# Kernel optimization log

Hardware: AMD Instinct MI355X
Metric: run time of the kernel (lower is better)

The kernel has to match this reference:

```python
import jax, jax.numpy as jnp
import numpy as np

N, D, DB, E, H = 1024, 512, 64, 32768, 1024

def setup_inputs() -> dict:
    key = jax.random.key(0)
    k = jax.random.split(key, 6)
    object_feats = jax.random.normal(k[0], (N, D), dtype=jnp.float32)
    bboxes_embedding = jax.random.normal(k[1], (N, N, DB), dtype=jnp.float32)
    pairs = jax.random.randint(k[2], (E, 2), 0, N, dtype=jnp.int64)
    # Kaiming-normal-ish init for the two Linear layers
    W1 = jax.random.normal(k[3], (D + D + DB, H), dtype=jnp.float32) * np.sqrt(2.0 / (D + D + DB))
    b1 = jnp.zeros((H,), dtype=jnp.float32)
    W2 = jax.random.normal(k[4], (H, D), dtype=jnp.float32) * np.sqrt(2.0 / H)
    b2 = jnp.zeros((D,), dtype=jnp.float32)
    return {"object_feats": object_feats, "bboxes_embedding": bboxes_embedding,
            "pairs": pairs, "W1": W1, "b1": b1, "W2": W2, "b2": b2}

def reference(object_feats, bboxes_embedding, pairs, W1, b1, W2, b2):
    sub = pairs[:, 0]
    obj = pairs[:, 1]
    # gather pair features: [E, D] each, plus pairwise bbox embedding [E, DB]
    f_sub = object_feats[sub]
    f_obj = object_feats[obj]
    bb = bboxes_embedding[sub, obj]
    x = jnp.concatenate((f_sub, f_obj, bb), axis=1)  # [E, 2D+DB]
    h = jax.nn.relu(x @ W1 + b1)
    out = h @ W2 + b2  # [E, D]
    n = object_feats.shape[0]
    # scatter-mean into subject nodes; each node's own feature is included once,
    # so new_feat[i] = (object_feats[i] + sum_{pairs with sub==i} out) / (1 + count[i]).
    # Nodes with no incident pairs keep their original feature (count==0 -> identity).
    seg_sum = jax.ops.segment_sum(out, sub, num_segments=n)  # [N, D]
    count = jax.ops.segment_sum(jnp.ones((out.shape[0],), dtype=out.dtype), sub, num_segments=n)
    new_feats = (object_feats + seg_sum) / (1.0 + count)[:, None]
    return (new_feats, bboxes_embedding, pairs)
```

## Files before the change

kernel.cpp:

```cpp
#include <hip/hip_runtime.h>

#define N_OBJ 1024
#define E_P   32768

typedef float f32x4 __attribute__((ext_vector_type(4)));
typedef short bf16x8 __attribute__((ext_vector_type(8)));
typedef unsigned short u16x4 __attribute__((ext_vector_type(4)));

__device__ __forceinline__ unsigned short f2bf(float f) {
    unsigned u = __float_as_uint(f);
    u = u + 0x7FFFu + ((u >> 16) & 1u);
    return (unsigned short)(u >> 16);
}

#define CP_OFF_PREP 0
#define CP_LEN_PREP 2097152
#define CP_OFF_PRE  (CP_OFF_PREP + CP_LEN_PREP)
#define CP_LEN_PRE  1048576
#define CP_OFF_PQ   (CP_OFF_PRE + CP_LEN_PRE)
#define CP_LEN_PQ   3145728
#define CP_OFF_SEG  (CP_OFF_PQ + CP_LEN_PQ)
#define CP_LEN_SEG  5242880
#define CP_OFF_OUT  (CP_OFF_SEG + CP_LEN_SEG)
#define CP_LEN_OUT  5242880

__device__ __forceinline__ void copy_role(const float4* __restrict__ src,
                                          float4* __restrict__ dst,
                                          int off, int len, int nblocks, int cb) {
    int i = off + cb * 256 + threadIdx.x;
    int end = off + len;
    int stride = nblocks * 256;
    for (; i < end; i += stride) dst[i] = src[i];
}

__global__ __launch_bounds__(256) void k_prep(const float* __restrict__ W1,
                                              const float* __restrict__ W2,
                                              const float* __restrict__ feats,
                                              unsigned short* __restrict__ w1pqT,
                                              unsigned short* __restrict__ w1cT,
                                              unsigned short* __restrict__ w2T,
                                              unsigned short* __restrict__ featsb,
                                              const float4* __restrict__ csrc,
                                              float4* __restrict__ cdst) {
    int bid = blockIdx.x;
    if ((bid % 3) == 2) { copy_role(csrc, cdst, CP_OFF_PREP, CP_LEN_PREP, 928, bid / 3); return; }
    int job = (bid / 3) * 2 + (bid % 3);
    int tid = threadIdx.x;
    if (job >= 1600) {
        int base = (job - 1600) * 2048 + tid * 8;
        float4 v0 = *(const float4*)&feats[base];
        float4 v1 = *(const float4*)&feats[base + 4];
        u16x4 o0 = { f2bf(v0.x), f2bf(v0.y), f2bf(v0.z), f2bf(v0.w) };
        u16x4 o1 = { f2bf(v1.x), f2bf(v1.y), f2bf(v1.z), f2bf(v1.w) };
        *(u16x4*)&featsb[base] = o0;
        *(u16x4*)&featsb[base + 4] = o1;
        return;
    }
    const float* in; unsigned short* out;
    int LDI, LDO, r0, c0, nbase, kbase;
    if (job < 1024) {
        int t = job; r0 = (t >> 5) * 32; c0 = (t & 31) * 32;
        in = W1; LDI = 1024; out = w1pqT; LDO = 512;
        nbase = c0 + (r0 >= 512 ? 1024 : 0); kbase = r0 & 511;
    } else if (job < 1088) {
        int t = job - 1024; r0 = 1024 + (t >> 5) * 32; c0 = (t & 31) * 32;
        in = W1; LDI = 1024; out = w1cT; LDO = 64;
        nbase = c0; kbase = r0 - 1024;
    } else {
        int t = job - 1088; r0 = (t >> 4) * 32; c0 = (t & 15) * 32;
        in = W2; LDI = 512; out = w2T; LDO = 1024;
        nbase = c0; kbase = r0;
    }
    __shared__ float lds[32][33];
    int ti = tid >> 3, tj = (tid & 7) * 4;
    float4 v = *(const float4*)&in[(size_t)(r0 + ti) * LDI + c0 + tj];
    lds[ti][tj] = v.x; lds[ti][tj + 1] = v.y; lds[ti][tj + 2] = v.z; lds[ti][tj + 3] = v.w;
    __syncthreads();
    int oc = tid >> 3, oj = (tid & 7) * 4;
    u16x4 o = { f2bf(lds[oj][oc]), f2bf(lds[oj + 1][oc]), f2bf(lds[oj + 2][oc]), f2bf(lds[oj + 3][oc]) };
    *(u16x4*)&out[(size_t)(nbase + oc) * LDO + kbase + oj] = o;
}

__global__ __launch_bounds__(256) void k_pre(const int* __restrict__ pairs,
                                             float* __restrict__ out_pairs,
                                             int* __restrict__ counts,
                                             const float4* __restrict__ csrc,
                                             float4* __restrict__ cdst) {
    int bid = blockIdx.x;
    if ((bid % 3) < 2) { copy_role(csrc, cdst, CP_OFF_PRE, CP_LEN_PRE, 512, (bid / 3) * 2 + (bid % 3)); return; }
    int i = (bid / 3) * 256 + threadIdx.x;
    if (i < 2 * E_P) out_pairs[i] = (float)pairs[i];
    if (i < E_P) atomicAdd(&counts[pairs[2 * i]], 1);
}

__global__ __launch_bounds__(256) void k_scan(const int* __restrict__ counts,
                                              int* __restrict__ offsets,
                                              int* __restrict__ cursor,
                                              int* __restrict__ brec,
                                              int* __restrict__ bcnt) {
    __shared__ int buf[2][256];
    int tid = threadIdx.x;
    int c[4]; int s = 0;
    #pragma unroll
    for (int i = 0; i < 4; ++i) { c[i] = counts[tid * 4 + i]; s += c[i]; }
    buf[0][tid] = s;
    __syncthreads();
    int sel = 0;
    for (int d = 1; d < 256; d <<= 1) {
        int v = buf[sel][tid];
        if (tid >= d) v += buf[sel][tid - d];
        buf[sel ^ 1][tid] = v;
        sel ^= 1;
        __syncthreads();
    }
    int base = buf[sel][tid] - s;
    int run = base;
    #pragma unroll
    for (int i = 0; i < 4; ++i) {
        offsets[tid * 4 + i] = run;
        cursor[tid * 4 + i]  = run;
        run += c[i];
    }
    if (tid == 255) offsets[1024] = run;
    int nb[4]; int t = 0;
    #pragma unroll
    for (int i = 0; i < 4; ++i) { nb[i] = (c[i] + 15) >> 4; t += nb[i]; }
    __syncthreads();
    buf[0][tid] = t;
    __syncthreads();
    sel = 0;
    for (int d = 1; d < 256; d <<= 1) {
        int v = buf[sel][tid];
        if (tid >= d) v += buf[sel][tid - d];
        buf[sel ^ 1][tid] = v;
        sel ^= 1;
        __syncthreads();
    }
    int bpos = buf[sel][tid] - t;
    #pragma unroll
    for (int i = 0; i < 4; ++i) {
        int seg = tid * 4 + i;
        for (int k = 0; k < nb[i]; ++k) brec[bpos++] = (seg << 8) | k;
    }
    if (tid == 255) bcnt[0] = bpos;
}

__global__ __launch_bounds__(256) void k_pq(const unsigned short* __restrict__ featsb,
                                            const unsigned short* __restrict__ w1pqT,
                                            const float* __restrict__ b1,
                                            float* __restrict__ P, float* __restrict__ Q,
                                            const int* __restrict__ pairs,
                                            int* __restrict__ cursor,
                                            int* __restrict__ csr,
                                            const float4* __restrict__ csrc,
                                            float4* __restrict__ cdst) {
    int bid = blockIdx.x;
    if (bid >= 1536) {
        int e = (bid - 1536) * 256 + threadIdx.x;
        if (e < E_P) {
            int sidx = pairs[2 * e];
            int pos = atomicAdd(&cursor[sidx], 1);
            csr[pos] = e;
        }
        return;
    }
    if ((bid % 3) < 2) { copy_role(csrc, cdst, CP_OFF_PQ, CP_LEN_PQ, 1024, (bid / 3) * 2 + (bid % 3)); return; }
    int job = bid / 3;
    int m0 = (job >> 5) * 64, n0 = (job & 31) * 64;
    int tid = threadIdx.x, w = tid >> 6, l = tid & 63;
    int ln = l & 15, kb = (l >> 4) * 8;
    int row = m0 + w * 16 + ln;
    f32x4 acc[4] = {};
    for (int k0 = 0; k0 < 512; k0 += 32) {
        bf16x8 a = *(const bf16x8*)&featsb[(size_t)row * 512 + k0 + kb];
        #pragma unroll
        for (int f = 0; f < 4; ++f) {
            bf16x8 b = *(const bf16x8*)&w1pqT[(size_t)(n0 + f * 16 + ln) * 512 + k0 + kb];
            acc[f] = __builtin_amdgcn_mfma_f32_16x16x32_bf16(a, b, acc[f], 0, 0, 0);
        }
    }
    int mr = m0 + w * 16 + (l >> 4) * 4;
    if (n0 < 1024) {
        #pragma unroll
        for (int f = 0; f < 4; ++f) {
            int n = n0 + f * 16 + ln;
            float b1v = b1[n];
            #pragma unroll
            for (int r = 0; r < 4; ++r)
                P[(size_t)(mr + r) * 1024 + n] = acc[f][r] + b1v;
        }
    } else {
        #pragma unroll
        for (int f = 0; f < 4; ++f) {
            int n = n0 - 1024 + f * 16 + ln;
            #pragma unroll
            for (int r = 0; r < 4; ++r)
                Q[(size_t)(mr + r) * 1024 + n] = acc[f][r];
        }
    }
}

__global__ __launch_bounds__(256) void k_seg(const int* __restrict__ csr,
                                             const int* __restrict__ offsets,
                                             const int* __restrict__ brec,
                                             const int* __restrict__ bcnt,
                                             const int* __restrict__ pairs,
                                             const float* __restrict__ bb,
                                             const unsigned short* __restrict__ w1cT,
                                             const float* __restrict__ P,
                                             const float* __restrict__ Q,
                                             float* __restrict__ HS,
                                             const float4* __restrict__ csrc,
                                             float4* __restrict__ cdst) {
    int bid = blockIdx.x;
    if ((bid % 3) == 0) { copy_role(csrc, cdst, CP_OFF_SEG, CP_LEN_SEG, 1536, bid / 3); return; }
    int b = (bid / 3) * 2 + (bid % 3) - 1;
    if (b >= bcnt[0]) return;
    int rec = brec[b];
    int seg = rec >> 8, kchunk = rec & 255;
    int start = offsets[seg] + kchunk * 16;
    int end = offsets[seg + 1];
    int n = end - start; if (n > 16) n = 16;

    const int tid = threadIdx.x, w = tid >> 6, l = tid & 63;
    const int ln = l & 15, g = l >> 4, kb = g * 8;
    const int n0 = w * 256;

    int idx = start + ln; int last = end - 1; if (idx > last) idx = last;
    int e = csr[idx];
    int obj = pairs[2 * e + 1];
    const float* br = &bb[((size_t)seg * 1024 + (size_t)obj) * 64];
    float4 a0 = *(const float4*)&br[kb];
    float4 a1 = *(const float4*)&br[kb + 4];
    float4 a2 = *(const float4*)&br[32 + kb];
    float4 a3 = *(const float4*)&br[32 + kb + 4];
    bf16x8 A0, A1;
    A0[0] = (short)f2bf(a0.x); A0[1] = (short)f2bf(a0.y); A0[2] = (short)f2bf(a0.z); A0[3] = (short)f2bf(a0.w);
    A0[4] = (short)f2bf(a1.x); A0[5] = (short)f2bf(a1.y); A0[6] = (short)f2bf(a1.z); A0[7] = (short)f2bf(a1.w);
    A1[0] = (short)f2bf(a2.x); A1[1] = (short)f2bf(a2.y); A1[2] = (short)f2bf(a2.z); A1[3] = (short)f2bf(a2.w);
    A1[4] = (short)f2bf(a3.x); A1[5] = (short)f2bf(a3.y); A1[6] = (short)f2bf(a3.z); A1[7] = (short)f2bf(a3.w);

    int ra0 = __shfl(obj, g * 4 + 0);
    int ra1 = __shfl(obj, g * 4 + 1);
    int ra2 = __shfl(obj, g * 4 + 2);
    int ra3 = __shfl(obj, g * 4 + 3);
    bool v0 = (g * 4 + 0) < n;
    bool v1 = (g * 4 + 1) < n;
    bool v2 = (g * 4 + 2) < n;
    bool v3 = (g * 4 + 3) < n;

    float pv[16];
    #pragma unroll
    for (int f = 0; f < 16; ++f)
        pv[f] = P[(size_t)seg * 1024 + n0 + f * 16 + ln];

    #pragma unroll
    for (int f = 0; f < 16; ++f) {
        const unsigned short* wr = &w1cT[(size_t)(n0 + f * 16 + ln) * 64];
        bf16x8 b0 = *(const bf16x8*)&wr[kb];
        bf16x8 b1v = *(const bf16x8*)&wr[32 + kb];
        f32x4 d = {0.f, 0.f, 0.f, 0.f};
        d = __builtin_amdgcn_mfma_f32_16x16x32_bf16(A0, b0, d, 0, 0, 0);
        d = __builtin_amdgcn_mfma_f32_16x16x32_bf16(A1, b1v, d, 0, 0, 0);
        int col = n0 + f * 16 + ln;
        float q0 = Q[(size_t)ra0 * 1024 + col];
        float q1 = Q[(size_t)ra1 * 1024 + col];
        float q2 = Q[(size_t)ra2 * 1024 + col];
        float q3 = Q[(size_t)ra3 * 1024 + col];
        float h = 0.f;
        h += v0 ? fmaxf(d[0] + pv[f] + q0, 0.f) : 0.f;
        h += v1 ? fmaxf(d[1] + pv[f] + q1, 0.f) : 0.f;
        h += v2 ? fmaxf(d[2] + pv[f] + q2, 0.f) : 0.f;
        h += v3 ? fmaxf(d[3] + pv[f] + q3, 0.f) : 0.f;
        h += __shfl_xor(h, 16);
        h += __shfl_xor(h, 32);
        if (l < 16) atomicAdd(&HS[(size_t)seg * 1024 + n0 + f * 16 + l], h);
    }
}

__global__ __launch_bounds__(256) void k_out(const float* __restrict__ HS,
                                             const unsigned short* __restrict__ w2T,
                                             const float* __restrict__ feats,
                                             const float* __restrict__ b2,
                                             const int* __restrict__ counts,
                                             float* __restrict__ out0,
                                             const float4* __restrict__ csrc,
                                             float4* __restrict__ cdst) {
    int bid = blockIdx.x;
    if ((bid % 13) != 12) { copy_role(csrc, cdst, CP_OFF_OUT, CP_LEN_OUT, 1536, (bid / 13) * 12 + (bid % 13)); return; }
    int job = bid / 13;
    int m0 = (job >> 3) * 64, n0 = (job & 7) * 64;
    int tid = threadIdx.x, w = tid >> 6, l = tid & 63;
    int ln = l & 15, kb = (l >> 4) * 8;
    int row = m0 + w * 16 + ln;
    f32x4 acc[4] = {};
    for (int k0 = 0; k0 < 1024; k0 += 32) {
        const float* hp = &HS[(size_t)row * 1024 + k0 + kb];
        float4 h0 = *(const float4*)&hp[0];
        float4 h1 = *(const float4*)&hp[4];
        bf16x8 a;
        a[0] = (short)f2bf(h0.x); a[1] = (short)f2bf(h0.y); a[2] = (short)f2bf(h0.z); a[3] = (short)f2bf(h0.w);
        a[4] = (short)f2bf(h1.x); a[5] = (short)f2bf(h1.y); a[6] = (short)f2bf(h1.z); a[7] = (short)f2bf(h1.w);
        #pragma unroll
        for (int f = 0; f < 4; ++f) {
            bf16x8 b = *(const bf16x8*)&w2T[(size_t)(n0 + f * 16 + ln) * 1024 + k0 + kb];
            acc[f] = __builtin_amdgcn_mfma_f32_16x16x32_bf16(a, b, acc[f], 0, 0, 0);
        }
    }
    int mr = m0 + w * 16 + (l >> 4) * 4;
    float cv[4], inv[4];
    #pragma unroll
    for (int r = 0; r < 4; ++r) {
        float c = (float)counts[mr + r];
        cv[r] = c;
        inv[r] = 1.0f / (1.0f + c);
    }
    #pragma unroll
    for (int f = 0; f < 4; ++f) {
        int n = n0 + f * 16 + ln;
        float b2v = b2[n];
        #pragma unroll
        for (int r = 0; r < 4; ++r) {
            float fv = feats[(size_t)(mr + r) * 512 + n];
            out0[(size_t)(mr + r) * 512 + n] = (fv + acc[f][r] + cv[r] * b2v) * inv[r];
        }
    }
}

extern "C" void kernel_launch(void* const* d_in, const int* in_sizes, int n_in,
                              void* d_out, int out_size, void* d_ws, size_t ws_size,
                              hipStream_t stream) {
    const float* feats = (const float*)d_in[0];
    const float* bb    = (const float*)d_in[1];
    const int*   pairs = (const int*)d_in[2];
    const float* W1    = (const float*)d_in[3];
    const float* b1    = (const float*)d_in[4];
    const float* W2    = (const float*)d_in[5];
    const float* b2    = (const float*)d_in[6];

    float* out        = (float*)d_out;
    float* out_feats  = out;
    float* out_bb     = out + (size_t)N_OBJ * 512;
    float* out_pairs  = out + (size_t)N_OBJ * 512 + (size_t)N_OBJ * N_OBJ * 64;

    char* w = (char*)d_ws;
    unsigned short* featsb = (unsigned short*)w;
    unsigned short* w1pqT  = (unsigned short*)(w + (1u << 20));
    float*          HS     = (float*)w;
    unsigned short* w1cT   = (unsigned short*)(w + (4u << 20));
    unsigned short* w2T    = (unsigned short*)(w + (4u << 20) + (128u << 10));
    float* P = (float*)(w + (5u << 20) + (128u << 10));
    float* Q = (float*)(w + (9u << 20) + (128u << 10));
    char* ints = w + (13u << 20) + (128u << 10);
    int* counts  = (int*)ints;
    int* offsets = (int*)(ints + 4096);
    int* cursor  = (int*)(ints + 12288);
    int* csr     = (int*)(ints + 16384);
    int* brec    = (int*)(ints + 16384 + 131072);
    int* bcnt    = (int*)(ints + 16384 + 131072 + 16384);

    const float4* cbb  = (const float4*)bb;
    float4*       cobb = (float4*)out_bb;

    hipMemsetAsync(counts, 0, 4096, stream);

    k_prep<<<2784, 256, 0, stream>>>(W1, W2, feats, w1pqT, w1cT, w2T, featsb, cbb, cobb);
    k_pre<<<768, 256, 0, stream>>>(pairs, out_pairs, counts, cbb, cobb);
    k_scan<<<1, 256, 0, stream>>>(counts, offsets, cursor, brec, bcnt);
    k_pq<<<1664, 256, 0, stream>>>(featsb, w1pqT, b1, P, Q, pairs, cursor, csr, cbb, cobb);

    hipMemsetAsync(HS, 0, (size_t)N_OBJ * 1024 * sizeof(float), stream);

    k_seg<<<4608, 256, 0, stream>>>(csr, offsets, brec, bcnt, pairs, bb, w1cT, P, Q, HS, cbb, cobb);
    k_out<<<1664, 256, 0, stream>>>(HS, w2T, feats, b2, counts, out_feats, cbb, cobb);
}
```

Before: 248.1 us.

## Fuse all stages into one cooperative persistent kernel with grid syncs

Replaces the six separate kernel launches and the HS memset with a single cooperative kernel. It runs persistent blocks, separates the stages with grid.sync, and splits blocks between compute jobs and the bulk bbox-embedding copy. It also stores subject-object indices directly in the CSR and packs start and count into the batch records, which removes the offsets and pairs lookups. The aim is to cut launch gaps and per-kernel tail effects. In exchange it adds grid-wide barriers and a fixed grid size that may limit parallelism in each phase.

```diff
diff --git a/kernel.cpp b/kernel.cpp
--- a/kernel.cpp
+++ b/kernel.cpp
@@ -1,4 +1,7 @@
 #include <hip/hip_runtime.h>
+#include <hip/hip_cooperative_groups.h>
+
+namespace cg = cooperative_groups;
 
 #define N_OBJ 1024
 #define E_P   32768
@@ -13,317 +16,306 @@
     return (unsigned short)(u >> 16);
 }
 
-#define CP_OFF_PREP 0
-#define CP_LEN_PREP 2097152
-#define CP_OFF_PRE  (CP_OFF_PREP + CP_LEN_PREP)
-#define CP_LEN_PRE  1048576
-#define CP_OFF_PQ   (CP_OFF_PRE + CP_LEN_PRE)
-#define CP_LEN_PQ   3145728
-#define CP_OFF_SEG  (CP_OFF_PQ + CP_LEN_PQ)
-#define CP_LEN_SEG  5242880
-#define CP_OFF_OUT  (CP_OFF_SEG + CP_LEN_SEG)
-#define CP_LEN_OUT  5242880
+#define LEN_A   1048576
+#define OFF_A   0
+#define LEN_B   393216
+#define OFF_B   (OFF_A + LEN_A)
+#define LEN_C   1048576
+#define OFF_C   (OFF_B + LEN_B)
+#define LEN_C2  393216
+#define OFF_C2  (OFF_C + LEN_C)
+#define LEN_D   1310720
+#define OFF_D   (OFF_C2 + LEN_C2)
+#define LEN_E   12582912
+#define OFF_E   (OFF_D + LEN_D)
+
+struct Params {
+    const float* feats; const float* bb; const int* pairs;
+    const float* W1; const float* b1; const float* W2; const float* b2;
+    float* out_feats; float* out_pairs;
+    const float4* csrc; float4* cdst;
+    unsigned short* featsb; unsigned short* w1pqT; unsigned short* w1cT; unsigned short* w2T;
+    float* P; float* Q; float* HS;
+    int* counts; int* cursor; int* csr_obj; unsigned* brec; int* bcnt;
+};
 
 __device__ __forceinline__ void copy_role(const float4* __restrict__ src,
                                           float4* __restrict__ dst,
-                                          int off, int len, int nblocks, int cb) {
+                                          int off, int len, int nb, int cb) {
+    int stride = nb * 256;
     int i = off + cb * 256 + threadIdx.x;
     int end = off + len;
-    int stride = nblocks * 256;
-    for (; i < end; i += stride) dst[i] = src[i];
+    for (; i + stride < end; i += 2 * stride) {
+        float4 a = src[i];
+        float4 b = src[i + stride];
+        dst[i] = a;
+        dst[i + stride] = b;
+    }
+    if (i < end) dst[i] = src[i];
 }
 
-__global__ __launch_bounds__(256) void k_prep(const float* __restrict__ W1,
-                                              const float* __restrict__ W2,
-                                              const float* __restrict__ feats,
-                                              unsigned short* __restrict__ w1pqT,
-                                              unsigned short* __restrict__ w1cT,
-                                              unsigned short* __restrict__ w2T,
-                                              unsigned short* __restrict__ featsb,
-                                              const float4* __restrict__ csrc,
-                                              float4* __restrict__ cdst) {
-    int bid = blockIdx.x;
-    if ((bid % 3) == 2) { copy_role(csrc, cdst, CP_OFF_PREP, CP_LEN_PREP, 928, bid / 3); return; }
-    int job = (bid / 3) * 2 + (bid % 3);
-    int tid = threadIdx.x;
-    if (job >= 1600) {
-        int base = (job - 1600) * 2048 + tid * 8;
-        float4 v0 = *(const float4*)&feats[base];
-        float4 v1 = *(const float4*)&feats[base + 4];
-        u16x4 o0 = { f2bf(v0.x), f2bf(v0.y), f2bf(v0.z), f2bf(v0.w) };
-        u16x4 o1 = { f2bf(v1.x), f2bf(v1.y), f2bf(v1.z), f2bf(v1.w) };
-        *(u16x4*)&featsb[base] = o0;
-        *(u16x4*)&featsb[base + 4] = o1;
-        return;
-    }
-    const float* in; unsigned short* out;
-    int LDI, LDO, r0, c0, nbase, kbase;
-    if (job < 1024) {
-        int t = job; r0 = (t >> 5) * 32; c0 = (t & 31) * 32;
-        in = W1; LDI = 1024; out = w1pqT; LDO = 512;
-        nbase = c0 + (r0 >= 512 ? 1024 : 0); kbase = r0 & 511;
-    } else if (job < 1088) {
-        int t = job - 1024; r0 = 1024 + (t >> 5) * 32; c0 = (t & 31) * 32;
-        in = W1; LDI = 1024; out = w1cT; LDO = 64;
-        nbase = c0; kbase = r0 - 1024;
-    } else {
-        int t = job - 1088; r0 = (t >> 4) * 32; c0 = (t & 15) * 32;
-        in = W2; LDI = 512; out = w2T; LDO = 1024;
-        nbase = c0; kbase = r0;
-    }
+__global__ __launch_bounds__(256, 3) void k_fused(Params p) {
+    cg::grid_group grid = cg::this_grid();
+    const int G = gridDim.x, bid = blockIdx.x, tid = threadIdx.x;
+    const int NC = G / 3;
+    const int GC = G - NC;
+
     __shared__ float lds[32][33];
-    int ti = tid >> 3, tj = (tid & 7) * 4;
-    float4 v = *(const float4*)&in[(size_t)(r0 + ti) * LDI + c0 + tj];
-    lds[ti][tj] = v.x; lds[ti][tj + 1] = v.y; lds[ti][tj + 2] = v.z; lds[ti][tj + 3] = v.w;
-    __syncthreads();
-    int oc = tid >> 3, oj = (tid & 7) * 4;
-    u16x4 o = { f2bf(lds[oj][oc]), f2bf(lds[oj + 1][oc]), f2bf(lds[oj + 2][oc]), f2bf(lds[oj + 3][oc]) };
-    *(u16x4*)&out[(size_t)(nbase + oc) * LDO + kbase + oj] = o;
-}
-
-__global__ __launch_bounds__(256) void k_pre(const int* __restrict__ pairs,
-                                             float* __restrict__ out_pairs,
-                                             int* __restrict__ counts,
-                                             const float4* __restrict__ csrc,
-                                             float4* __restrict__ cdst) {
-    int bid = blockIdx.x;
-    if ((bid % 3) < 2) { copy_role(csrc, cdst, CP_OFF_PRE, CP_LEN_PRE, 512, (bid / 3) * 2 + (bid % 3)); return; }
-    int i = (bid / 3) * 256 + threadIdx.x;
-    if (i < 2 * E_P) out_pairs[i] = (float)pairs[i];
-    if (i < E_P) atomicAdd(&counts[pairs[2 * i]], 1);
-}
-
-__global__ __launch_bounds__(256) void k_scan(const int* __restrict__ counts,
-                                              int* __restrict__ offsets,
-                                              int* __restrict__ cursor,
-                                              int* __restrict__ brec,
-                                              int* __restrict__ bcnt) {
     __shared__ int buf[2][256];
-    int tid = threadIdx.x;
-    int c[4]; int s = 0;
-    #pragma unroll
-    for (int i = 0; i < 4; ++i) { c[i] = counts[tid * 4 + i]; s += c[i]; }
-    buf[0][tid] = s;
-    __syncthreads();
-    int sel = 0;
-    for (int d = 1; d < 256; d <<= 1) {
-        int v = buf[sel][tid];
-        if (tid >= d) v += buf[sel][tid - d];
-        buf[sel ^ 1][tid] = v;
-        sel ^= 1;
+
+    if (bid < GC) {
+        for (int job = bid; job < 2112; job += GC) {
+            if (job >= 1856) {
+                int i = (job - 1856) * 256 + tid;
+                p.out_pairs[i] = (float)p.pairs[i];
+                if (i < E_P) atomicAdd(&p.counts[p.pairs[2 * i]], 1);
+            } else if (job >= 1600) {
+                int base = (job - 1600) * 2048 + tid * 8;
+                float4 v0 = *(const float4*)&p.feats[base];
+                float4 v1 = *(const float4*)&p.feats[base + 4];
+                u16x4 o0 = { f2bf(v0.x), f2bf(v0.y), f2bf(v0.z), f2bf(v0.w) };
+                u16x4 o1 = { f2bf(v1.x), f2bf(v1.y), f2bf(v1.z), f2bf(v1.w) };
+                *(u16x4*)&p.featsb[base] = o0;
+                *(u16x4*)&p.featsb[base + 4] = o1;
+            } else {
+                const float* in; unsigned short* out;
+                int LDI, LDO, r0, c0, nbase, kbase;
+                if (job < 1024) {
+                    r0 = (job >> 5) * 32; c0 = (job & 31) * 32;
+                    in = p.W1; LDI = 1024; out = p.w1pqT; LDO = 512;
+                    nbase = c0 + (r0 >= 512 ? 1024 : 0); kbase = r0 & 511;
+                } else if (job < 1088) {
+                    int t = job - 1024; r0 = 1024 + (t >> 5) * 32; c0 = (t & 31) * 32;
+                    in = p.W1; LDI = 1024; out = p.w1cT; LDO = 64;
+                    nbase = c0; kbase = r0 - 1024;
+                } else {
+                    int t = job - 1088; r0 = (t >> 4) * 32; c0 = (t & 15) * 32;
+                    in = p.W2; LDI = 512; out = p.w2T; LDO = 1024;
+                    nbase = c0; kbase = r0;
+                }
+                __syncthreads();
+                int ti = tid >> 3, tj = (tid & 7) * 4;
+                float4 v = *(const float4*)&in[(size_t)(r0 + ti) * LDI + c0 + tj];
+                lds[ti][tj] = v.x; lds[ti][tj + 1] = v.y; lds[ti][tj + 2] = v.z; lds[ti][tj + 3] = v.w;
+                __syncthreads();
+                int oc = tid >> 3, oj = (tid & 7) * 4;
+                u16x4 o = { f2bf(lds[oj][oc]), f2bf(lds[oj + 1][oc]),
+                            f2bf(lds[oj + 2][oc]), f2bf(lds[oj + 3][oc]) };
+                *(u16x4*)&out[(size_t)(nbase + oc) * LDO + kbase + oj] = o;
+            }
+        }
+    } else {
+        copy_role(p.csrc, p.cdst, OFF_A, LEN_A, NC, bid - GC);
+    }
+    grid.sync();
+
+    if (bid == 0) {
+        int c[4]; int s = 0;
+        #pragma unroll
+        for (int i = 0; i < 4; ++i) { c[i] = p.counts[tid * 4 + i]; s += c[i]; }
+        buf[0][tid] = s;
         __syncthreads();
-    }
-    int base = buf[sel][tid] - s;
-    int run = base;
-    #pragma unroll
-    for (int i = 0; i < 4; ++i) {
-        offsets[tid * 4 + i] = run;
-        cursor[tid * 4 + i]  = run;
-        run += c[i];
-    }
-    if (tid == 255) offsets[1024] = run;
-    int nb[4]; int t = 0;
-    #pragma unroll
-    for (int i = 0; i < 4; ++i) { nb[i] = (c[i] + 15) >> 4; t += nb[i]; }
-    __syncthreads();
-    buf[0][tid] = t;
-    __syncthreads();
-    sel = 0;
-    for (int d = 1; d < 256; d <<= 1) {
-        int v = buf[sel][tid];
-        if (tid >= d) v += buf[sel][tid - d];
-        buf[sel ^ 1][tid] = v;
-        sel ^= 1;
+        int sel = 0;
+        for (int d = 1; d < 256; d <<= 1) {
+            int v = buf[sel][tid];
+            if (tid >= d) v += buf[sel][tid - d];
+            buf[sel ^ 1][tid] = v;
+            sel ^= 1;
+            __syncthreads();
+        }
+        int base = buf[sel][tid] - s;
+        int run = base;
+        #pragma unroll
+        for (int i = 0; i < 4; ++i) { p.cursor[tid * 4 + i] = run; run += c[i]; }
+        int nb[4]; int t = 0;
+        #pragma unroll
+        for (int i = 0; i < 4; ++i) { nb[i] = (c[i] + 15) >> 4; t += nb[i]; }
         __syncthreads();
-    }
-    int bpos = buf[sel][tid] - t;
-    #pragma unroll
-    for (int i = 0; i < 4; ++i) {
-        int seg = tid * 4 + i;
-        for (int k = 0; k < nb[i]; ++k) brec[bpos++] = (seg << 8) | k;
-    }
-    if (tid == 255) bcnt[0] = bpos;
-}
-
-__global__ __launch_bounds__(256) void k_pq(const unsigned short* __restrict__ featsb,
-                                            const unsigned short* __restrict__ w1pqT,
-                                            const float* __restrict__ b1,
-                                            float* __restrict__ P, float* __restrict__ Q,
-                                            const int* __restrict__ pairs,
-                                            int* __restrict__ cursor,
-                                            int* __restrict__ csr,
-                                            const float4* __restrict__ csrc,
-                                            float4* __restrict__ cdst) {
-    int bid = blockIdx.x;
-    if (bid >= 1536) {
-        int e = (bid - 1536) * 256 + threadIdx.x;
-        if (e < E_P) {
-            int sidx = pairs[2 * e];
-            int pos = atomicAdd(&cursor[sidx], 1);
-            csr[pos] = e;
-        }
-        return;
-    }
-    if ((bid % 3) < 2) { copy_role(csrc, cdst, CP_OFF_PQ, CP_LEN_PQ, 1024, (bid / 3) * 2 + (bid % 3)); return; }
-    int job = bid / 3;
-    int m0 = (job >> 5) * 64, n0 = (job & 31) * 64;
-    int tid = threadIdx.x, w = tid >> 6, l = tid & 63;
-    int ln = l & 15, kb = (l >> 4) * 8;
-    int row = m0 + w * 16 + ln;
-    f32x4 acc[4] = {};
-    for (int k0 = 0; k0 < 512; k0 += 32) {
-        bf16x8 a = *(const bf16x8*)&featsb[(size_t)row * 512 + k0 + kb];
+        buf[0][tid] = t;
+        __syncthreads();
+        sel = 0;
+        for (int d = 1; d < 256; d <<= 1) {
+            int v = buf[sel][tid];
+            if (tid >= d) v += buf[sel][tid - d];
+            buf[sel ^ 1][tid] = v;
+            sel ^= 1;
+            __syncthreads();
+        }
+        int bpos = buf[sel][tid] - t;
+        int run2 = base;
+        #pragma unroll
+        for (int i = 0; i < 4; ++i) {
+            int seg = tid * 4 + i;
+            for (int k = 0; k < nb[i]; ++k) {
+                int st = run2 + k * 16;
+                int cnt = c[i] - k * 16; if (cnt > 16) cnt = 16;
+                p.brec[bpos++] = (unsigned)st | ((unsigned)seg << 16) | ((unsigned)(cnt - 1) << 26);
+            }
+            run2 += c[i];
+        }
+        if (tid == 255) p.bcnt[0] = bpos;
+    } else {
+        copy_role(p.csrc, p.cdst, OFF_B, LEN_B, G - 1, bid - 1);
+    }
+    grid.sync();
+
+    if (bid < GC) {
+        for (int job = bid; job < 640; job += GC) {
+            if (job < 128) {
+                int e = job * 256 + tid;
+                int sidx = p.pairs[2 * e];
+                int pos = atomicAdd(&p.cursor[sidx], 1);
+                p.csr_obj[pos] = p.pairs[2 * e + 1];
+            } else {
+                int t = job - 128;
+                int m0 = (t >> 5) * 64, n0 = (t & 31) * 64;
+                int w = tid >> 6, l = tid & 63;
+                int ln = l & 15, kb = (l >> 4) * 8;
+                int row = m0 + w * 16 + ln;
+                f32x4 acc[4] = {};
+                for (int k0 = 0; k0 < 512; k0 += 32) {
+                    bf16x8 a = *(const bf16x8*)&p.featsb[(size_t)row * 512 + k0 + kb];
+                    #pragma unroll
+                    for (int f = 0; f < 4; ++f) {
+                        bf16x8 b = *(const bf16x8*)&p.w1pqT[(size_t)(n0 + f * 16 + ln) * 512 + k0 + kb];
+                        acc[f] = __builtin_amdgcn_mfma_f32_16x16x32_bf16(a, b, acc[f], 0, 0, 0);
+                    }
+                }
+                int mr = m0 + w * 16 + (l >> 4) * 4;
+                if (n0 < 1024) {
+                    #pragma unroll
+                    for (int f = 0; f < 4; ++f) {
+                        int n = n0 + f * 16 + ln;
+                        float b1v = p.b1[n];
+                        #pragma unroll
+                        for (int r = 0; r < 4; ++r)
+                            p.P[(size_t)(mr + r) * 1024 + n] = acc[f][r] + b1v;
+                    }
+                } else {
+                    #pragma unroll
+                    for (int f = 0; f < 4; ++f) {
+                        int n = n0 - 1024 + f * 16 + ln;
+                        #pragma unroll
+                        for (int r = 0; r < 4; ++r)
+                            p.Q[(size_t)(mr + r) * 1024 + n] = acc[f][r];
+                    }
+                }
+            }
+        }
+    } else {
+        copy_role(p.csrc, p.cdst, OFF_C, LEN_C, NC, bid - GC);
+    }
+    grid.sync();
+
+    {
+        float4 z = make_float4(0.f, 0.f, 0.f, 0.f);
+        float4* hs4 = (float4*)p.HS;
+        for (int i = bid * 256 + tid; i < 262144; i += G * 256) hs4[i] = z;
+        copy_role(p.csrc, p.cdst, OFF_C2, LEN_C2, G, bid);
+    }
+    grid.sync();
+
+    if (bid < GC) {
+        const int nbatch = p.bcnt[0];
+        const int w = tid >> 6, l = tid & 63;
+        const int ln = l & 15, g4 = l >> 4, kb = g4 * 8;
+        const int n0 = w * 256;
+        for (int j = bid; j < nbatch; j += GC) {
+            unsigned rec = p.brec[j];
+            int start = rec & 0xFFFF;
+            int seg = (rec >> 16) & 0x3FF;
+            int n = ((rec >> 26) & 15) + 1;
+
+            int idx = start + (ln < n ? ln : n - 1);
+            int obj = p.csr_obj[idx];
+            const float* br = &p.bb[((size_t)seg * 1024 + (size_t)obj) * 64];
+            float4 a0 = *(const float4*)&br[kb];
+            float4 a1 = *(const float4*)&br[kb + 4];
+            float4 a2 = *(const float4*)&br[32 + kb];
+            float4 a3 = *(const float4*)&br[32 + kb + 4];
+            bf16x8 A0, A1;
+            A0[0] = (short)f2bf(a0.x); A0[1] = (short)f2bf(a0.y); A0[2] = (short)f2bf(a0.z); A0[3] = (short)f2bf(a0.w);
+            A0[4] = (short)f2bf(a1.x); A0[5] = (short)f2bf(a1.y); A0[6] = (short)f2bf(a1.z); A0[7] = (short)f2bf(a1.w);
+            A1[0] = (short)f2bf(a2.x); A1[1] = (short)f2bf(a2.y); A1[2] = (short)f2bf(a2.z); A1[3] = (short)f2bf(a2.w);
+            A1[4] = (short)f2bf(a3.x); A1[5] = (short)f2bf(a3.y); A1[6] = (short)f2bf(a3.z); A1[7] = (short)f2bf(a3.w);
+
+            int ra0 = __shfl(obj, g4 * 4 + 0);
+            int ra1 = __shfl(obj, g4 * 4 + 1);
+            int ra2 = __shfl(obj, g4 * 4 + 2);
+            int ra3 = __shfl(obj, g4 * 4 + 3);
+            bool v0 = (g4 * 4 + 0) < n;
+            bool v1 = (g4 * 4 + 1) < n;
+            bool v2 = (g4 * 4 + 2) < n;
+            bool v3 = (g4 * 4 + 3) < n;
+
+            #pragma unroll
+            for (int f = 0; f < 16; ++f) {
+                float pv = p.P[(size_t)seg * 1024 + n0 + f * 16 + ln];
+                const unsigned short* wr = &p.w1cT[(size_t)(n0 + f * 16 + ln) * 64];
+                bf16x8 b0 = *(const bf16x8*)&wr[kb];
+                bf16x8 b1 = *(const bf16x8*)&wr[32 + kb];
+                f32x4 d = {0.f, 0.f, 0.f, 0.f};
+                d = __builtin_amdgcn_mfma_f32_16x16x32_bf16(A0, b0, d, 0, 0, 0);
+                d = __builtin_amdgcn_mfma_f32_16x16x32_bf16(A1, b1, d, 0, 0, 0);
+                int col = n0 + f * 16 + ln;
+                float q0 = p.Q[(size_t)ra0 * 1024 + col];
+                float q1 = p.Q[(size_t)ra1 * 1024 + col];
+                float q2 = p.Q[(size_t)ra2 * 1024 + col];
+                float q3 = p.Q[(size_t)ra3 * 1024 + col];
+                float h = 0.f;
+                h += v0 ? fmaxf(d[0] + pv + q0, 0.f) : 0.f;
+                h += v1 ? fmaxf(d[1] + pv + q1, 0.f) : 0.f;
+                h += v2 ? fmaxf(d[2] + pv + q2, 0.f) : 0.f;
+                h += v3 ? fmaxf(d[3] + pv + q3, 0.f) : 0.f;
+                h += __shfl_xor(h, 16);
+                h += __shfl_xor(h, 32);
+                if (l < 16) atomicAdd(&p.HS[(size_t)seg * 1024 + n0 + f * 16 + l], h);
+            }
+        }
+    } else {
+        copy_role(p.csrc, p.cdst, OFF_D, LEN_D, NC, bid - GC);
+    }
+    grid.sync();
+
+    if (bid < 128) {
+        int m0 = (bid >> 3) * 64, n0 = (bid & 7) * 64;
+        int w = tid >> 6, l = tid & 63;
+        int ln = l & 15, kb = (l >> 4) * 8;
+        int row = m0 + w * 16 + ln;
+        f32x4 acc[4] = {};
+        for (int k0 = 0; k0 < 1024; k0 += 32) {
+            const float* hp = &p.HS[(size_t)row * 1024 + k0 + kb];
+            float4 h0 = *(const float4*)&hp[0];
+            float4 h1 = *(const float4*)&hp[4];
+            bf16x8 a;
+            a[0] = (short)f2bf(h0.x); a[1] = (short)f2bf(h0.y); a[2] = (short)f2bf(h0.z); a[3] = (short)f2bf(h0.w);
+            a[4] = (short)f2bf(h1.x); a[5] = (short)f2bf(h1.y); a[6] = (short)f2bf(h1.z); a[7] = (short)f2bf(h1.w);
+            #pragma unroll
+            for (int f = 0; f < 4; ++f) {
+                bf16x8 b = *(const bf16x8*)&p.w2T[(size_t)(n0 + f * 16 + ln) * 1024 + k0 + kb];
+                acc[f] = __builtin_amdgcn_mfma_f32_16x16x32_bf16(a, b, acc[f], 0, 0, 0);
+            }
+        }
+        int mr = m0 + w * 16 + (l >> 4) * 4;
+        float cv[4], inv[4];
+        #pragma unroll
+        for (int r = 0; r < 4; ++r) {
+            float c = (float)p.counts[mr + r];
+            cv[r] = c;
+            inv[r] = 1.0f / (1.0f + c);
+        }
         #pragma unroll
         for (int f = 0; f < 4; ++f) {
-            bf16x8 b = *(const bf16x8*)&w1pqT[(size_t)(n0 + f * 16 + ln) * 512 + k0 + kb];
-            acc[f] = __builtin_amdgcn_mfma_f32_16x16x32_bf16(a, b, acc[f], 0, 0, 0);
-        }
-    }
-    int mr = m0 + w * 16 + (l >> 4) * 4;
-    if (n0 < 1024) {
-        #pragma unroll
-        for (int f = 0; f < 4; ++f) {
-            int n = n0 + f * 16 + ln;
-            float b1v = b1[n];
+            int nn = n0 + f * 16 + ln;
+            float b2v = p.b2[nn];
             #pragma unroll
-            for (int r = 0; r < 4; ++r)
-                P[(size_t)(mr + r) * 1024 + n] = acc[f][r] + b1v;
-        }
-    } else {
-        #pragma unroll
-        for (int f = 0; f < 4; ++f) {
-            int n = n0 - 1024 + f * 16 + ln;
-            #pragma unroll
-            for (int r = 0; r < 4; ++r)
-                Q[(size_t)(mr + r) * 1024 + n] = acc[f][r];
-        }
-    }
-}
-
-__global__ __launch_bounds__(256) void k_seg(const int* __restrict__ csr,
-                                             const int* __restrict__ offsets,
-                                             const int* __restrict__ brec,
-                                             const int* __restrict__ bcnt,
-                                             const int* __restrict__ pairs,
-                                             const float* __restrict__ bb,
-                                             const unsigned short* __restrict__ w1cT,
-                                             const float* __restrict__ P,
-                                             const float* __restrict__ Q,
-                                             float* __restrict__ HS,
-                                             const float4* __restrict__ csrc,
-                                             float4* __restrict__ cdst) {
-    int bid = blockIdx.x;
-    if ((bid % 3) == 0) { copy_role(csrc, cdst, CP_OFF_SEG, CP_LEN_SEG, 1536, bid / 3); return; }
-    int b = (bid / 3) * 2 + (bid % 3) - 1;
-    if (b >= bcnt[0]) return;
-    int rec = brec[b];
-    int seg = rec >> 8, kchunk = rec & 255;
-    int start = offsets[seg] + kchunk * 16;
-    int end = offsets[seg + 1];
-    int n = end - start; if (n > 16) n = 16;
-
-    const int tid = threadIdx.x, w = tid >> 6, l = tid & 63;
-    const int ln = l & 15, g = l >> 4, kb = g * 8;
-    const int n0 = w * 256;
-
-    int idx = start + ln; int last = end - 1; if (idx > last) idx = last;
-    int e = csr[idx];
-    int obj = pairs[2 * e + 1];
-    const float* br = &bb[((size_t)seg * 1024 + (size_t)obj) * 64];
-    float4 a0 = *(const float4*)&br[kb];
-    float4 a1 = *(const float4*)&br[kb + 4];
-    float4 a2 = *(const float4*)&br[32 + kb];
-    float4 a3 = *(const float4*)&br[32 + kb + 4];
-    bf16x8 A0, A1;
-    A0[0] = (short)f2bf(a0.x); A0[1] = (short)f2bf(a0.y); A0[2] = (short)f2bf(a0.z); A0[3] = (short)f2bf(a0.w);
-    A0[4] = (short)f2bf(a1.x); A0[5] = (short)f2bf(a1.y); A0[6] = (short)f2bf(a1.z); A0[7] = (short)f2bf(a1.w);
-    A1[0] = (short)f2bf(a2.x); A1[1] = (short)f2bf(a2.y); A1[2] = (short)f2bf(a2.z); A1[3] = (short)f2bf(a2.w);
-    A1[4] = (short)f2bf(a3.x); A1[5] = (short)f2bf(a3.y); A1[6] = (short)f2bf(a3.z); A1[7] = (short)f2bf(a3.w);
-
-    int ra0 = __shfl(obj, g * 4 + 0);
-    int ra1 = __shfl(obj, g * 4 + 1);
-    int ra2 = __shfl(obj, g * 4 + 2);
-    int ra3 = __shfl(obj, g * 4 + 3);
-    bool v0 = (g * 4 + 0) < n;
-    bool v1 = (g * 4 + 1) < n;
-    bool v2 = (g * 4 + 2) < n;
-    bool v3 = (g * 4 + 3) < n;
-
-    float pv[16];
-    #pragma unroll
-    for (int f = 0; f < 16; ++f)
-        pv[f] = P[(size_t)seg * 1024 + n0 + f * 16 + ln];
-
-    #pragma unroll
-    for (int f = 0; f < 16; ++f) {
-        const unsigned short* wr = &w1cT[(size_t)(n0 + f * 16 + ln) * 64];
-        bf16x8 b0 = *(const bf16x8*)&wr[kb];
-        bf16x8 b1v = *(const bf16x8*)&wr[32 + kb];
-        f32x4 d = {0.f, 0.f, 0.f, 0.f};
-        d = __builtin_amdgcn_mfma_f32_16x16x32_bf16(A0, b0, d, 0, 0, 0);
-        d = __builtin_amdgcn_mfma_f32_16x16x32_bf16(A1, b1v, d, 0, 0, 0);
-        int col = n0 + f * 16 + ln;
-        float q0 = Q[(size_t)ra0 * 1024 + col];
-        float q1 = Q[(size_t)ra1 * 1024 + col];
-        float q2 = Q[(size_t)ra2 * 1024 + col];
-        float q3 = Q[(size_t)ra3 * 1024 + col];
-        float h = 0.f;
-        h += v0 ? fmaxf(d[0] + pv[f] + q0, 0.f) : 0.f;
-        h += v1 ? fmaxf(d[1] + pv[f] + q1, 0.f) : 0.f;
-        h += v2 ? fmaxf(d[2] + pv[f] + q2, 0.f) : 0.f;
-        h += v3 ? fmaxf(d[3] + pv[f] + q3, 0.f) : 0.f;
-        h += __shfl_xor(h, 16);
-        h += __shfl_xor(h, 32);
-        if (l < 16) atomicAdd(&HS[(size_t)seg * 1024 + n0 + f * 16 + l], h);
-    }
-}
-
-__global__ __launch_bounds__(256) void k_out(const float* __restrict__ HS,
-                                             const unsigned short* __restrict__ w2T,
-                                             const float* __restrict__ feats,
-                                             const float* __restrict__ b2,
-                                             const int* __restrict__ counts,
-                                             float* __restrict__ out0,
-                                             const float4* __restrict__ csrc,
-                                             float4* __restrict__ cdst) {
-    int bid = blockIdx.x;
-    if ((bid % 13) != 12) { copy_role(csrc, cdst, CP_OFF_OUT, CP_LEN_OUT, 1536, (bid / 13) * 12 + (bid % 13)); return; }
-    int job = bid / 13;
-    int m0 = (job >> 3) * 64, n0 = (job & 7) * 64;
-    int tid = threadIdx.x, w = tid >> 6, l = tid & 63;
-    int ln = l & 15, kb = (l >> 4) * 8;
-    int row = m0 + w * 16 + ln;
-    f32x4 acc[4] = {};
-    for (int k0 = 0; k0 < 1024; k0 += 32) {
-        const float* hp = &HS[(size_t)row * 1024 + k0 + kb];
-        float4 h0 = *(const float4*)&hp[0];
-        float4 h1 = *(const float4*)&hp[4];
-        bf16x8 a;
-        a[0] = (short)f2bf(h0.x); a[1] = (short)f2bf(h0.y); a[2] = (short)f2bf(h0.z); a[3] = (short)f2bf(h0.w);
-        a[4] = (short)f2bf(h1.x); a[5] = (short)f2bf(h1.y); a[6] = (short)f2bf(h1.z); a[7] = (short)f2bf(h1.w);
-        #pragma unroll
-        for (int f = 0; f < 4; ++f) {
-            bf16x8 b = *(const bf16x8*)&w2T[(size_t)(n0 + f * 16 + ln) * 1024 + k0 + kb];
-            acc[f] = __builtin_amdgcn_mfma_f32_16x16x32_bf16(a, b, acc[f], 0, 0, 0);
-        }
-    }
-    int mr = m0 + w * 16 + (l >> 4) * 4;
-    float cv[4], inv[4];
-    #pragma unroll
-    for (int r = 0; r < 4; ++r) {
-        float c = (float)counts[mr + r];
-        cv[r] = c;
-        inv[r] = 1.0f / (1.0f + c);
-    }
-    #pragma unroll
-    for (int f = 0; f < 4; ++f) {
-        int n = n0 + f * 16 + ln;
-        float b2v = b2[n];
-        #pragma unroll
-        for (int r = 0; r < 4; ++r) {
-            float fv = feats[(size_t)(mr + r) * 512 + n];
-            out0[(size_t)(mr + r) * 512 + n] = (fv + acc[f][r] + cv[r] * b2v) * inv[r];
-        }
+            for (int r = 0; r < 4; ++r) {
+                float fv = p.feats[(size_t)(mr + r) * 512 + nn];
+                p.out_feats[(size_t)(mr + r) * 512 + nn] = (fv + acc[f][r] + cv[r] * b2v) * inv[r];
+            }
+        }
+    } else {
+        copy_role(p.csrc, p.cdst, OFF_E, LEN_E, G - 128, bid - 128);
     }
 }
 
@@ -344,33 +336,34 @@
     float* out_pairs  = out + (size_t)N_OBJ * 512 + (size_t)N_OBJ * N_OBJ * 64;
 
     char* w = (char*)d_ws;
-    unsigned short* featsb = (unsigned short*)w;
-    unsigned short* w1pqT  = (unsigned short*)(w + (1u << 20));
-    float*          HS     = (float*)w;
-    unsigned short* w1cT   = (unsigned short*)(w + (4u << 20));
-    unsigned short* w2T    = (unsigned short*)(w + (4u << 20) + (128u << 10));
-    float* P = (float*)(w + (5u << 20) + (128u << 10));
-    float* Q = (float*)(w + (9u << 20) + (128u << 10));
+    Params p;
+    p.feats = feats; p.bb = bb; p.pairs = pairs;
+    p.W1 = W1; p.b1 = b1; p.W2 = W2; p.b2 = b2;
+    p.out_feats = out_feats; p.out_pairs = out_pairs;
+    p.csrc = (const float4*)bb; p.cdst = (float4*)out_bb;
+    p.featsb = (unsigned short*)w;
+    p.w1pqT  = (unsigned short*)(w + (1u << 20));
+    p.HS     = (float*)w;
+    p.w1cT   = (unsigned short*)(w + (4u << 20));
+    p.w2T    = (unsigned short*)(w + (4u << 20) + (128u << 10));
+    p.P      = (float*)(w + (5u << 20) + (128u << 10));
+    p.Q      = (float*)(w + (9u << 20) + (128u << 10));
     char* ints = w + (13u << 20) + (128u << 10);
-    int* counts  = (int*)ints;
-    int* offsets = (int*)(ints + 4096);
-    int* cursor  = (int*)(ints + 12288);
-    int* csr     = (int*)(ints + 16384);
-    int* brec    = (int*)(ints + 16384 + 131072);
-    int* bcnt    = (int*)(ints + 16384 + 131072 + 16384);
-
-    const float4* cbb  = (const float4*)bb;
-    float4*       cobb = (float4*)out_bb;
-
-    hipMemsetAsync(counts, 0, 4096, stream);
-
-    k_prep<<<2784, 256, 0, stream>>>(W1, W2, feats, w1pqT, w1cT, w2T, featsb, cbb, cobb);
-    k_pre<<<768, 256, 0, stream>>>(pairs, out_pairs, counts, cbb, cobb);
-    k_scan<<<1, 256, 0, stream>>>(counts, offsets, cursor, brec, bcnt);
-    k_pq<<<1664, 256, 0, stream>>>(featsb, w1pqT, b1, P, Q, pairs, cursor, csr, cbb, cobb);
-
-    hipMemsetAsync(HS, 0, (size_t)N_OBJ * 1024 * sizeof(float), stream);
-
-    k_seg<<<4608, 256, 0, stream>>>(csr, offsets, brec, bcnt, pairs, bb, w1cT, P, Q, HS, cbb, cobb);
-    k_out<<<1664, 256, 0, stream>>>(HS, w2T, feats, b2, counts, out_feats, cbb, cobb);
+    p.counts  = (int*)ints;
+    p.cursor  = (int*)(ints + 4096);
+    p.csr_obj = (int*)(ints + 8192);
+    p.brec    = (unsigned*)(ints + 8192 + 131072);
+    p.bcnt    = (int*)(ints + 8192 + 131072 + 16384);
+
+    hipMemsetAsync(p.counts, 0, 4096, stream);
+
+    int bpc = 0;
+    hipError_t oe = hipOccupancyMaxActiveBlocksPerMultiprocessor(&bpc, (const void*)k_fused, 256, 0);
+    if (oe != hipSuccess || bpc < 1) bpc = 2;
+    int G = bpc * 256;
+    if (G > 1024) G = 1024;
+    if (G < 256)  G = 256;
+
+    void* args[] = { (void*)&p };
+    hipLaunchCooperativeKernel((const void*)k_fused, dim3(G), dim3(256), args, 0, stream);
 }
```

Measured after the change: 566.0 us. 2.28x slower.
